# Optimization experiments

Measured on AMD Instinct MI355X. Metric: run time of the kernel, lower is better.

Reference implementation:

```python
import jax, jax.numpy as jnp
import numpy as np

HEADS = 16
EMBED = 1024
HEAD_DIM = EMBED // HEADS


def setup_inputs() -> dict:
    key = jax.random.key(0)
    ks = jax.random.split(key, 7)
    B, S, E = 2, 2048, EMBED
    scale = 1.0 / np.sqrt(E)
    return {
        "query": jax.random.normal(ks[0], (B, S, E), dtype=jnp.float32),
        "key": jax.random.normal(ks[1], (B, S, E), dtype=jnp.float32),
        "value": jax.random.normal(ks[2], (B, S, E), dtype=jnp.float32),
        # nn.Linear(E, E, bias=False) weights, applied as x @ W.T
        "Wq": jax.random.normal(ks[3], (E, E), dtype=jnp.float32) * scale,
        "Wk": jax.random.normal(ks[4], (E, E), dtype=jnp.float32) * scale,
        "Wv": jax.random.normal(ks[5], (E, E), dtype=jnp.float32) * scale,
        "Wo": jax.random.normal(ks[6], (E, E), dtype=jnp.float32) * scale,
    }


def reference(query, key, value, Wq, Wk, Wv, Wo):
    B, S, E = query.shape
    H, D = HEADS, HEAD_DIM

    def split_heads(x, W):
        # [B,S,E] @ W.T -> [B,S,E] -> [B,H,S,D]
        return (x @ W.T).reshape(B, -1, H, D).transpose(0, 2, 1, 3)

    q = split_heads(query, Wq)
    k = split_heads(key, Wk)
    v = split_heads(value, Wv)

    scores = jnp.einsum("bhqd,bhkd->bhqk", q, k) / jnp.sqrt(jnp.float32(D))
    attn = jax.nn.softmax(scores, axis=-1)  # [B,H,S,S]
    x = jnp.einsum("bhqk,bhkd->bhqd", attn, v)
    x = x.transpose(0, 2, 1, 3).reshape(B, -1, H * D)
    return x @ Wo.T
```

## Files before the change

kernel.cpp:

```cpp
#include <hip/hip_runtime.h>
#include <hip/hip_bf16.h>


typedef __attribute__((ext_vector_type(8))) short short8;
typedef __attribute__((ext_vector_type(4))) float f32x4;
typedef __attribute__((ext_vector_type(4))) unsigned short us4;
typedef __attribute__((ext_vector_type(4))) int i32x4;

#define MFMA16(a, b, c) __builtin_amdgcn_mfma_f32_16x16x32_bf16(a, b, c, 0, 0, 0)

static constexpr int B = 2;
static constexpr int S = 2048;
static constexpr int E = 1024;
static constexpr int H = 16;
static constexpr int D = 64;
static constexpr int M = B * S;
static constexpr size_t NE = (size_t)M * E;
static constexpr size_t NW = (size_t)E * E;

static __device__ __forceinline__ unsigned short f2bf(float x) {
  unsigned int u = __float_as_uint(x);
  unsigned int r = (u + 0x7FFFu + ((u >> 16) & 1u)) >> 16;
  return (unsigned short)r;
}

static __device__ __forceinline__ int cvt_pk_bf16(float lo, float hi) {
  int r;
  asm("v_cvt_pk_bf16_f32 %0, %1, %2" : "=v"(r) : "v"(lo), "v"(hi));
  return r;
}

static __device__ __forceinline__ void gload_lds16(const unsigned short* g,
                                                   unsigned short* l) {
  __builtin_amdgcn_global_load_lds(
      (const __attribute__((address_space(1))) unsigned int*)g,
      (__attribute__((address_space(3))) unsigned int*)l, 16, 0, 0);
}

__global__ void cvt_act_kernel(const float* __restrict__ s0,
                               const float* __restrict__ s1,
                               const float* __restrict__ s2,
                               unsigned short* __restrict__ d0,
                               unsigned short* __restrict__ d1,
                               unsigned short* __restrict__ d2, int n4) {
  const float* src = (blockIdx.y == 0) ? s0 : ((blockIdx.y == 1) ? s1 : s2);
  unsigned short* dst = (blockIdx.y == 0) ? d0 : ((blockIdx.y == 1) ? d1 : d2);
  for (int i = blockIdx.x * blockDim.x + threadIdx.x; i < n4;
       i += gridDim.x * blockDim.x) {
    float4 v = reinterpret_cast<const float4*>(src)[i];
    ushort4 o;
    o.x = f2bf(v.x); o.y = f2bf(v.y); o.z = f2bf(v.z); o.w = f2bf(v.w);
    reinterpret_cast<ushort4*>(dst)[i] = o;
  }
}

__global__ void cvt_w_kernel(const float* __restrict__ s0,
                             const float* __restrict__ s1,
                             const float* __restrict__ s2,
                             const float* __restrict__ s3,
                             unsigned short* __restrict__ d0,
                             unsigned short* __restrict__ d1,
                             unsigned short* __restrict__ d2,
                             unsigned short* __restrict__ d3, int n4) {
  const int z = blockIdx.y;
  const float* src = (z == 0) ? s0 : ((z == 1) ? s1 : ((z == 2) ? s2 : s3));
  unsigned short* dst = (z == 0) ? d0 : ((z == 1) ? d1 : ((z == 2) ? d2 : d3));
  for (int i = blockIdx.x * blockDim.x + threadIdx.x; i < n4;
       i += gridDim.x * blockDim.x) {
    float4 v = reinterpret_cast<const float4*>(src)[i];
    ushort4 o;
    o.x = f2bf(v.x); o.y = f2bf(v.y); o.z = f2bf(v.z); o.w = f2bf(v.w);
    reinterpret_cast<ushort4*>(dst)[i] = o;
  }
}

__global__ __launch_bounds__(256) void gemm_proj_kernel(
    const unsigned short* __restrict__ xq, const unsigned short* __restrict__ xk,
    const unsigned short* __restrict__ xv, const unsigned short* __restrict__ wq,
    const unsigned short* __restrict__ wk, const unsigned short* __restrict__ wv,
    unsigned short* __restrict__ Qh, unsigned short* __restrict__ Kh,
    unsigned short* __restrict__ Vt) {
  __shared__ __align__(16) unsigned short As[2][128 * 32];
  __shared__ __align__(16) unsigned short Bs[2][128 * 32];

  const int which = blockIdx.z;
  const unsigned short* A = (which == 0) ? xq : ((which == 1) ? xk : xv);
  const unsigned short* W = (which == 0) ? wq : ((which == 1) ? wk : wv);

  const int wave = threadIdx.x >> 6;
  const int lane = threadIdx.x & 63;
  const int lr = lane & 15;
  const int lk = (lane >> 4) * 8;
  const int m0 = blockIdx.x * 128;
  const int n0 = blockIdx.y * 128;
  const int wm = (wave >> 1) * 64;
  const int wn = (wave & 1) * 64;
  const int srow = lane >> 2;
  const int scol = (lane & 3) * 8;

  f32x4 acc[4][4];
  const f32x4 fz = {0.f, 0.f, 0.f, 0.f};
#pragma unroll
  for (int i = 0; i < 4; ++i)
#pragma unroll
    for (int j = 0; j < 4; ++j) acc[i][j] = fz;

#define STAGE_G(bb, kk)                                                       \
  {                                                                           \
    _Pragma("unroll") for (int i = 0; i < 2; ++i) {                           \
      const int c = wave * 2 + i;                                             \
      const int row = c * 16 + srow;                                          \
      gload_lds16(A + (size_t)(m0 + row) * E + (kk) + scol, &As[bb][c * 512]);\
      gload_lds16(W + (size_t)(n0 + row) * E + (kk) + scol, &Bs[bb][c * 512]);\
    }                                                                         \
  }

  STAGE_G(0, 0);
  __syncthreads();
  int buf = 0;
  for (int kk = 0; kk < E; kk += 32) {
    if (kk + 32 < E) STAGE_G(buf ^ 1, kk + 32);
    short8 af[4], bw[4];
#pragma unroll
    for (int i = 0; i < 4; ++i)
      af[i] = *reinterpret_cast<const short8*>(
          &As[buf][(wm + i * 16 + lr) * 32 + lk]);
#pragma unroll
    for (int j = 0; j < 4; ++j)
      bw[j] = *reinterpret_cast<const short8*>(
          &Bs[buf][(wn + j * 16 + lr) * 32 + lk]);
#pragma unroll
    for (int i = 0; i < 4; ++i)
#pragma unroll
      for (int j = 0; j < 4; ++j) acc[i][j] = MFMA16(af[i], bw[j], acc[i][j]);
    __syncthreads();
    buf ^= 1;
  }
#undef STAGE_G

  const int rbase = (lane >> 4) * 4;
#pragma unroll
  for (int i = 0; i < 4; ++i) {
#pragma unroll
    for (int j = 0; j < 4; ++j) {
      const int col = n0 + wn + j * 16 + lr;
      const int h = col >> 6, d = col & 63;
#pragma unroll
      for (int r = 0; r < 4; ++r) {
        const int row = m0 + wm + i * 16 + rbase + r;
        const int b = row >> 11, s = row & (S - 1);
        const float v = acc[i][j][r];
        if (which == 0) {
          Qh[(((size_t)b * H + h) * S + s) * D + d] = f2bf(v * 0.18033688f);
        } else if (which == 1) {
          Kh[(((size_t)b * H + h) * S + s) * D + d] = f2bf(v);
        } else {
          Vt[(((size_t)b * H + h) * D + d) * S + s] = f2bf(v);
        }
      }
    }
  }
}

__global__ __launch_bounds__(256) void gemm_out_kernel(
    const unsigned short* __restrict__ X, const unsigned short* __restrict__ Wo,
    float* __restrict__ out) {
  __shared__ __align__(16) unsigned short As[2][128 * 32];
  __shared__ __align__(16) unsigned short Bs[2][64 * 32];

  const int wave = threadIdx.x >> 6;
  const int lane = threadIdx.x & 63;
  const int lr = lane & 15;
  const int lk = (lane >> 4) * 8;
  const int m0 = blockIdx.x * 128;
  const int n0 = blockIdx.y * 64;
  const int wm = (wave >> 1) * 64;
  const int wn = (wave & 1) * 32;
  const int srow = lane >> 2;
  const int scol = (lane & 3) * 8;

  f32x4 acc[4][2];
  const f32x4 fz = {0.f, 0.f, 0.f, 0.f};
#pragma unroll
  for (int i = 0; i < 4; ++i)
#pragma unroll
    for (int j = 0; j < 2; ++j) acc[i][j] = fz;

#define STAGE_O(bb, kk)                                                       \
  {                                                                           \
    _Pragma("unroll") for (int i = 0; i < 2; ++i) {                           \
      const int c = wave * 2 + i;                                             \
      const int row = c * 16 + srow;                                          \
      gload_lds16(X + (size_t)(m0 + row) * E + (kk) + scol, &As[bb][c * 512]);\
    }                                                                         \
    gload_lds16(Wo + (size_t)(n0 + wave * 16 + srow) * E + (kk) + scol,       \
                &Bs[bb][wave * 512]);                                         \
  }

  STAGE_O(0, 0);
  __syncthreads();
  int buf = 0;
  for (int kk = 0; kk < E; kk += 32) {
    if (kk + 32 < E) STAGE_O(buf ^ 1, kk + 32);
    short8 af[4], bw[2];
#pragma unroll
    for (int i = 0; i < 4; ++i)
      af[i] = *reinterpret_cast<const short8*>(
          &As[buf][(wm + i * 16 + lr) * 32 + lk]);
#pragma unroll
    for (int j = 0; j < 2; ++j)
      bw[j] = *reinterpret_cast<const short8*>(
          &Bs[buf][(wn + j * 16 + lr) * 32 + lk]);
#pragma unroll
    for (int i = 0; i < 4; ++i)
#pragma unroll
      for (int j = 0; j < 2; ++j) acc[i][j] = MFMA16(af[i], bw[j], acc[i][j]);
    __syncthreads();
    buf ^= 1;
  }
#undef STAGE_O

  const int rbase = (lane >> 4) * 4;
#pragma unroll
  for (int i = 0; i < 4; ++i) {
#pragma unroll
    for (int j = 0; j < 2; ++j) {
      const int col = n0 + wn + j * 16 + lr;
#pragma unroll
      for (int r = 0; r < 4; ++r) {
        const int row = m0 + wm + i * 16 + rbase + r;
        out[(size_t)row * E + col] = acc[i][j][r];
      }
    }
  }
}

__global__ __launch_bounds__(256) void attn_kernel(
    const unsigned short* __restrict__ Qh, const unsigned short* __restrict__ Kh,
    const unsigned short* __restrict__ Vt, unsigned short* __restrict__ Xb) {
  __shared__ __align__(16) unsigned short Ks[2][64 * 64];
  __shared__ __align__(16) unsigned short Vs[2][64 * 64];

  const int wave = threadIdx.x >> 6;
  const int lane = threadIdx.x & 63;
  const int lr = lane & 15;
  const int jj = lane >> 4;
  const int lk = jj * 8;

  const int lin = blockIdx.x + (blockIdx.y << 5);
  const int nlin = (lin & 7) * 128 + (lin >> 3);
  const int qt = nlin & 31;
  const int bh = nlin >> 5;
  const int q0 = qt * 64 + wave * 16;

  const unsigned short* Qp = Qh + ((size_t)bh * S + q0) * D;
  short8 qf0 = *reinterpret_cast<const short8*>(Qp + (size_t)lr * D + lk);
  short8 qf1 = *reinterpret_cast<const short8*>(Qp + (size_t)lr * D + 32 + lk);

  const unsigned short* Kbase = Kh + (size_t)bh * S * D;
  const unsigned short* Vbase = Vt + (size_t)bh * D * S;

  const f32x4 fz = {0.f, 0.f, 0.f, 0.f};
  float mrun = -3.0e38f, lsum = 0.f;
  f32x4 acc[4];
#pragma unroll
  for (int dt = 0; dt < 4; ++dt) acc[dt] = fz;

  const int srow = lane >> 3;
  const int sgV = (lane & 7) ^ srow;

#define STAGE_KV(bb, kt)                                                      \
  {                                                                           \
    _Pragma("unroll") for (int i = 0; i < 2; ++i) {                           \
      const int c = wave * 2 + i;                                             \
      const int sgK = (lane & 7) ^ ((srow & 3) | ((c & 1) << 2));             \
      gload_lds16(Kbase + (size_t)((kt) + c * 8 + srow) * D + sgK * 8,        \
                  &Ks[bb][c * 512]);                                          \
      gload_lds16(Vbase + (size_t)(c * 8 + srow) * S + (kt) + sgV * 8,        \
                  &Vs[bb][c * 512]);                                          \
    }                                                                         \
  }

  STAGE_KV(0, 0);
  __syncthreads();
  int buf = 0;

  const int rb = ((lr >> 2) << 3) + (lr & 3);
  const int kswz = (lr & 3) | (((lr >> 2) & 1) << 2);
  const int vswz = lr & 7;

  constexpr int NT = S / 64;
  for (int t = 0; t < NT; ++t) {
    if (t + 1 < NT) STAGE_KV(buf ^ 1, (t + 1) * 64);

    f32x4 sf[4];
    __builtin_amdgcn_s_setprio(1);
#pragma unroll
    for (int nt = 0; nt < 4; ++nt) {
      const int r = rb + ((nt & 1) << 2) + ((nt >> 1) << 5);
      short8 kf0 = *reinterpret_cast<const short8*>(
          &Ks[buf][r * 64 + ((jj ^ kswz) * 8)]);
      short8 kf1 = *reinterpret_cast<const short8*>(
          &Ks[buf][r * 64 + (((jj + 4) ^ kswz) * 8)]);
      f32x4 z = fz;
      z = MFMA16(kf0, qf0, z);
      z = MFMA16(kf1, qf1, z);
      sf[nt] = z;
    }
    __builtin_amdgcn_s_setprio(0);

    short8 vf0[4], vf1[4];
#pragma unroll
    for (int dt = 0; dt < 4; ++dt) {
      const int r = dt * 16 + lr;
      vf0[dt] = *reinterpret_cast<const short8*>(
          &Vs[buf][r * 64 + ((jj ^ vswz) * 8)]);
      vf1[dt] = *reinterpret_cast<const short8*>(
          &Vs[buf][r * 64 + (((jj + 4) ^ vswz) * 8)]);
    }

    float mx = sf[0][0];
#pragma unroll
    for (int nt = 0; nt < 4; ++nt)
#pragma unroll
      for (int r = 0; r < 4; ++r) mx = fmaxf(mx, sf[nt][r]);
    mx = fmaxf(mx, __shfl_xor(mx, 16));
    mx = fmaxf(mx, __shfl_xor(mx, 32));

    if (__any(mx > mrun + 8.f)) {
      const float nm = fmaxf(mrun, mx);
      const float fac = __builtin_amdgcn_exp2f(mrun - nm);
      mrun = nm;
      lsum *= fac;
#pragma unroll
      for (int dt = 0; dt < 4; ++dt)
#pragma unroll
        for (int r = 0; r < 4; ++r) acc[dt][r] *= fac;
    }

    float p[4][4];
#pragma unroll
    for (int nt = 0; nt < 4; ++nt)
#pragma unroll
      for (int r = 0; r < 4; ++r) {
        p[nt][r] = __builtin_amdgcn_exp2f(sf[nt][r] - mrun);
        lsum += p[nt][r];
      }
    i32x4 w0, w1;
    w0.x = cvt_pk_bf16(p[0][0], p[0][1]);
    w0.y = cvt_pk_bf16(p[0][2], p[0][3]);
    w0.z = cvt_pk_bf16(p[1][0], p[1][1]);
    w0.w = cvt_pk_bf16(p[1][2], p[1][3]);
    w1.x = cvt_pk_bf16(p[2][0], p[2][1]);
    w1.y = cvt_pk_bf16(p[2][2], p[2][3]);
    w1.z = cvt_pk_bf16(p[3][0], p[3][1]);
    w1.w = cvt_pk_bf16(p[3][2], p[3][3]);
    short8 pa0 = __builtin_bit_cast(short8, w0);
    short8 pa1 = __builtin_bit_cast(short8, w1);

    __builtin_amdgcn_s_setprio(1);
#pragma unroll
    for (int dt = 0; dt < 4; ++dt) {
      acc[dt] = MFMA16(vf0[dt], pa0, acc[dt]);
      acc[dt] = MFMA16(vf1[dt], pa1, acc[dt]);
    }
    __builtin_amdgcn_s_setprio(0);

    __syncthreads();
    buf ^= 1;
  }
#undef STAGE_KV

  float ltot = lsum;
  ltot += __shfl_xor(ltot, 16);
  ltot += __shfl_xor(ltot, 32);
  const float inv = 1.0f / ltot;
  const int b = bh >> 4, h = bh & (H - 1);
  const int row = q0 + lr;
#pragma unroll
  for (int dt = 0; dt < 4; ++dt) {
    us4 o;
#pragma unroll
    for (int r = 0; r < 4; ++r) o[r] = f2bf(acc[dt][r] * inv);
    *reinterpret_cast<us4*>(
        &Xb[((size_t)b * S + row) * E + h * D + dt * 16 + 4 * jj]) = o;
  }
}

extern "C" void kernel_launch(void* const* d_in, const int* in_sizes, int n_in,
                              void* d_out, int out_size, void* d_ws, size_t ws_size,
                              hipStream_t stream) {
  const float* q_f = (const float*)d_in[0];
  const float* k_f = (const float*)d_in[1];
  const float* v_f = (const float*)d_in[2];
  const float* wq_f = (const float*)d_in[3];
  const float* wk_f = (const float*)d_in[4];
  const float* wv_f = (const float*)d_in[5];
  const float* wo_f = (const float*)d_in[6];

  unsigned short* xq = (unsigned short*)d_ws;
  unsigned short* xk = xq + NE;
  unsigned short* xv = xk + NE;
  unsigned short* wq = xv + NE;
  unsigned short* wk = wq + NW;
  unsigned short* wv = wk + NW;
  unsigned short* wo = wv + NW;
  unsigned short* Qh = wo + NW;
  unsigned short* Kh = Qh + NE;
  unsigned short* Vt = Kh + NE;
  unsigned short* Xb = Vt + NE;

  cvt_act_kernel<<<dim3(512, 3), 256, 0, stream>>>(q_f, k_f, v_f, xq, xk, xv,
                                                   (int)(NE / 4));
  cvt_w_kernel<<<dim3(256, 4), 256, 0, stream>>>(wq_f, wk_f, wv_f, wo_f, wq, wk,
                                                 wv, wo, (int)(NW / 4));

  gemm_proj_kernel<<<dim3(M / 128, E / 128, 3), 256, 0, stream>>>(
      xq, xk, xv, wq, wk, wv, Qh, Kh, Vt);

  attn_kernel<<<dim3(S / 64, B * H), 256, 0, stream>>>(Qh, Kh, Vt, Xb);

  gemm_out_kernel<<<dim3(M / 128, E / 64), 256, 0, stream>>>(Xb, wo,
                                                             (float*)d_out);
}
```

Before: 159.5 us.

## Process two 16-row query tiles per wave in attention to reuse K/V fragments

Each wave of the attention kernel now handles 32 query rows as two independent 16-row tiles, so the block covers 128 queries and the grid in x is halved. K and V fragments read from LDS are reused across both tiles, and the global K/V staging per query row is also halved. Each tile keeps its own softmax state. The cost is roughly double the accumulator and score registers and only 512 blocks, which may lower occupancy and the number of waves in flight.

```diff
diff --git a/kernel.cpp b/kernel.cpp
--- a/kernel.cpp
+++ b/kernel.cpp
@@ -247,24 +247,28 @@
   const int jj = lane >> 4;
   const int lk = jj * 8;
 
-  const int lin = blockIdx.x + (blockIdx.y << 5);
-  const int nlin = (lin & 7) * 128 + (lin >> 3);
-  const int qt = nlin & 31;
-  const int bh = nlin >> 5;
-  const int q0 = qt * 64 + wave * 16;
-
-  const unsigned short* Qp = Qh + ((size_t)bh * S + q0) * D;
-  short8 qf0 = *reinterpret_cast<const short8*>(Qp + (size_t)lr * D + lk);
-  short8 qf1 = *reinterpret_cast<const short8*>(Qp + (size_t)lr * D + 32 + lk);
+  const int lin = blockIdx.x + (blockIdx.y << 4);
+  const int nlin = (lin & 7) * 64 + (lin >> 3);
+  const int qt = nlin & 15;
+  const int bh = nlin >> 4;
+  const int q0 = qt * 128 + wave * 32;
+
+  const unsigned short* Qp0 = Qh + ((size_t)bh * S + q0) * D;
+  const unsigned short* Qp1 = Qp0 + (size_t)16 * D;
+  short8 qa0 = *reinterpret_cast<const short8*>(Qp0 + (size_t)lr * D + lk);
+  short8 qa1 = *reinterpret_cast<const short8*>(Qp0 + (size_t)lr * D + 32 + lk);
+  short8 qb0 = *reinterpret_cast<const short8*>(Qp1 + (size_t)lr * D + lk);
+  short8 qb1 = *reinterpret_cast<const short8*>(Qp1 + (size_t)lr * D + 32 + lk);
 
   const unsigned short* Kbase = Kh + (size_t)bh * S * D;
   const unsigned short* Vbase = Vt + (size_t)bh * D * S;
 
   const f32x4 fz = {0.f, 0.f, 0.f, 0.f};
-  float mrun = -3.0e38f, lsum = 0.f;
-  f32x4 acc[4];
-#pragma unroll
-  for (int dt = 0; dt < 4; ++dt) acc[dt] = fz;
+  float mrunA = -3.0e38f, lsumA = 0.f;
+  float mrunB = -3.0e38f, lsumB = 0.f;
+  f32x4 accA[4], accB[4];
+#pragma unroll
+  for (int dt = 0; dt < 4; ++dt) { accA[dt] = fz; accB[dt] = fz; }
 
   const int srow = lane >> 3;
   const int sgV = (lane & 7) ^ srow;
@@ -293,7 +297,7 @@
   for (int t = 0; t < NT; ++t) {
     if (t + 1 < NT) STAGE_KV(buf ^ 1, (t + 1) * 64);
 
-    f32x4 sf[4];
+    f32x4 sfA[4], sfB[4];
     __builtin_amdgcn_s_setprio(1);
 #pragma unroll
     for (int nt = 0; nt < 4; ++nt) {
@@ -302,10 +306,13 @@
           &Ks[buf][r * 64 + ((jj ^ kswz) * 8)]);
       short8 kf1 = *reinterpret_cast<const short8*>(
           &Ks[buf][r * 64 + (((jj + 4) ^ kswz) * 8)]);
-      f32x4 z = fz;
-      z = MFMA16(kf0, qf0, z);
-      z = MFMA16(kf1, qf1, z);
-      sf[nt] = z;
+      f32x4 za = fz, zb = fz;
+      za = MFMA16(kf0, qa0, za);
+      za = MFMA16(kf1, qa1, za);
+      zb = MFMA16(kf0, qb0, zb);
+      zb = MFMA16(kf1, qb1, zb);
+      sfA[nt] = za;
+      sfB[nt] = zb;
     }
     __builtin_amdgcn_s_setprio(0);
 
@@ -319,50 +326,87 @@
           &Vs[buf][r * 64 + (((jj + 4) ^ vswz) * 8)]);
     }
 
-    float mx = sf[0][0];
+    float mxA = sfA[0][0];
 #pragma unroll
     for (int nt = 0; nt < 4; ++nt)
 #pragma unroll
-      for (int r = 0; r < 4; ++r) mx = fmaxf(mx, sf[nt][r]);
-    mx = fmaxf(mx, __shfl_xor(mx, 16));
-    mx = fmaxf(mx, __shfl_xor(mx, 32));
-
-    if (__any(mx > mrun + 8.f)) {
-      const float nm = fmaxf(mrun, mx);
-      const float fac = __builtin_amdgcn_exp2f(mrun - nm);
-      mrun = nm;
-      lsum *= fac;
+      for (int r = 0; r < 4; ++r) mxA = fmaxf(mxA, sfA[nt][r]);
+    mxA = fmaxf(mxA, __shfl_xor(mxA, 16));
+    mxA = fmaxf(mxA, __shfl_xor(mxA, 32));
+    if (__any(mxA > mrunA + 8.f)) {
+      const float nm = fmaxf(mrunA, mxA);
+      const float fac = __builtin_amdgcn_exp2f(mrunA - nm);
+      mrunA = nm;
+      lsumA *= fac;
 #pragma unroll
       for (int dt = 0; dt < 4; ++dt)
 #pragma unroll
-        for (int r = 0; r < 4; ++r) acc[dt][r] *= fac;
-    }
-
-    float p[4][4];
+        for (int r = 0; r < 4; ++r) accA[dt][r] *= fac;
+    }
+    float pA[4][4];
 #pragma unroll
     for (int nt = 0; nt < 4; ++nt)
 #pragma unroll
       for (int r = 0; r < 4; ++r) {
-        p[nt][r] = __builtin_amdgcn_exp2f(sf[nt][r] - mrun);
-        lsum += p[nt][r];
+        pA[nt][r] = __builtin_amdgcn_exp2f(sfA[nt][r] - mrunA);
+        lsumA += pA[nt][r];
       }
-    i32x4 w0, w1;
-    w0.x = cvt_pk_bf16(p[0][0], p[0][1]);
-    w0.y = cvt_pk_bf16(p[0][2], p[0][3]);
-    w0.z = cvt_pk_bf16(p[1][0], p[1][1]);
-    w0.w = cvt_pk_bf16(p[1][2], p[1][3]);
-    w1.x = cvt_pk_bf16(p[2][0], p[2][1]);
-    w1.y = cvt_pk_bf16(p[2][2], p[2][3]);
-    w1.z = cvt_pk_bf16(p[3][0], p[3][1]);
-    w1.w = cvt_pk_bf16(p[3][2], p[3][3]);
-    short8 pa0 = __builtin_bit_cast(short8, w0);
-    short8 pa1 = __builtin_bit_cast(short8, w1);
+    i32x4 wa0, wa1;
+    wa0.x = cvt_pk_bf16(pA[0][0], pA[0][1]);
+    wa0.y = cvt_pk_bf16(pA[0][2], pA[0][3]);
+    wa0.z = cvt_pk_bf16(pA[1][0], pA[1][1]);
+    wa0.w = cvt_pk_bf16(pA[1][2], pA[1][3]);
+    wa1.x = cvt_pk_bf16(pA[2][0], pA[2][1]);
+    wa1.y = cvt_pk_bf16(pA[2][2], pA[2][3]);
+    wa1.z = cvt_pk_bf16(pA[3][0], pA[3][1]);
+    wa1.w = cvt_pk_bf16(pA[3][2], pA[3][3]);
+    short8 paA0 = __builtin_bit_cast(short8, wa0);
+    short8 paA1 = __builtin_bit_cast(short8, wa1);
+
+    float mxB = sfB[0][0];
+#pragma unroll
+    for (int nt = 0; nt < 4; ++nt)
+#pragma unroll
+      for (int r = 0; r < 4; ++r) mxB = fmaxf(mxB, sfB[nt][r]);
+    mxB = fmaxf(mxB, __shfl_xor(mxB, 16));
+    mxB = fmaxf(mxB, __shfl_xor(mxB, 32));
+    if (__any(mxB > mrunB + 8.f)) {
+      const float nm = fmaxf(mrunB, mxB);
+      const float fac = __builtin_amdgcn_exp2f(mrunB - nm);
+      mrunB = nm;
+      lsumB *= fac;
+#pragma unroll
+      for (int dt = 0; dt < 4; ++dt)
+#pragma unroll
+        for (int r = 0; r < 4; ++r) accB[dt][r] *= fac;
+    }
+    float pB[4][4];
+#pragma unroll
+    for (int nt = 0; nt < 4; ++nt)
+#pragma unroll
+      for (int r = 0; r < 4; ++r) {
+        pB[nt][r] = __builtin_amdgcn_exp2f(sfB[nt][r] - mrunB);
+        lsumB += pB[nt][r];
+      }
+    i32x4 wb0, wb1;
+    wb0.x = cvt_pk_bf16(pB[0][0], pB[0][1]);
+    wb0.y = cvt_pk_bf16(pB[0][2], pB[0][3]);
+    wb0.z = cvt_pk_bf16(pB[1][0], pB[1][1]);
+    wb0.w = cvt_pk_bf16(pB[1][2], pB[1][3]);
+    wb1.x = cvt_pk_bf16(pB[2][0], pB[2][1]);
+    wb1.y = cvt_pk_bf16(pB[2][2], pB[2][3]);
+    wb1.z = cvt_pk_bf16(pB[3][0], pB[3][1]);
+    wb1.w = cvt_pk_bf16(pB[3][2], pB[3][3]);
+    short8 paB0 = __builtin_bit_cast(short8, wb0);
+    short8 paB1 = __builtin_bit_cast(short8, wb1);
 
     __builtin_amdgcn_s_setprio(1);
 #pragma unroll
     for (int dt = 0; dt < 4; ++dt) {
-      acc[dt] = MFMA16(vf0[dt], pa0, acc[dt]);
-      acc[dt] = MFMA16(vf1[dt], pa1, acc[dt]);
+      accA[dt] = MFMA16(vf0[dt], paA0, accA[dt]);
+      accA[dt] = MFMA16(vf1[dt], paA1, accA[dt]);
+      accB[dt] = MFMA16(vf0[dt], paB0, accB[dt]);
+      accB[dt] = MFMA16(vf1[dt], paB1, accB[dt]);
     }
     __builtin_amdgcn_s_setprio(0);
 
@@ -371,19 +415,36 @@
   }
 #undef STAGE_KV
 
-  float ltot = lsum;
-  ltot += __shfl_xor(ltot, 16);
-  ltot += __shfl_xor(ltot, 32);
-  const float inv = 1.0f / ltot;
   const int b = bh >> 4, h = bh & (H - 1);
-  const int row = q0 + lr;
-#pragma unroll
-  for (int dt = 0; dt < 4; ++dt) {
-    us4 o;
-#pragma unroll
-    for (int r = 0; r < 4; ++r) o[r] = f2bf(acc[dt][r] * inv);
-    *reinterpret_cast<us4*>(
-        &Xb[((size_t)b * S + row) * E + h * D + dt * 16 + 4 * jj]) = o;
+  {
+    float ltot = lsumA;
+    ltot += __shfl_xor(ltot, 16);
+    ltot += __shfl_xor(ltot, 32);
+    const float inv = 1.0f / ltot;
+    const int row = q0 + lr;
+#pragma unroll
+    for (int dt = 0; dt < 4; ++dt) {
+      us4 o;
+#pragma unroll
+      for (int r = 0; r < 4; ++r) o[r] = f2bf(accA[dt][r] * inv);
+      *reinterpret_cast<us4*>(
+          &Xb[((size_t)b * S + row) * E + h * D + dt * 16 + 4 * jj]) = o;
+    }
+  }
+  {
+    float ltot = lsumB;
+    ltot += __shfl_xor(ltot, 16);
+    ltot += __shfl_xor(ltot, 32);
+    const float inv = 1.0f / ltot;
+    const int row = q0 + 16 + lr;
+#pragma unroll
+    for (int dt = 0; dt < 4; ++dt) {
+      us4 o;
+#pragma unroll
+      for (int r = 0; r < 4; ++r) o[r] = f2bf(accB[dt][r] * inv);
+      *reinterpret_cast<us4*>(
+          &Xb[((size_t)b * S + row) * E + h * D + dt * 16 + 4 * jj]) = o;
+    }
   }
 }
 
@@ -418,7 +479,7 @@
   gemm_proj_kernel<<<dim3(M / 128, E / 128, 3), 256, 0, stream>>>(
       xq, xk, xv, wq, wk, wv, Qh, Kh, Vt);
 
-  attn_kernel<<<dim3(S / 64, B * H), 256, 0, stream>>>(Qh, Kh, Vt, Xb);
+  attn_kernel<<<dim3(S / 128, B * H), 256, 0, stream>>>(Qh, Kh, Vt, Xb);
 
   gemm_out_kernel<<<dim3(M / 128, E / 64), 256, 0, stream>>>(Xb, wo,
                                                              (float*)d_out);
```

Result: faster. 145.4 us (-8.8%).

## Give each attention wave four query tiles to reuse K/V fragments; merge conversion kernels

Applied to the files above, without the earlier changes.

The attention kernel now runs 2 waves per block, each handling 64 query rows (four 16-row groups) instead of 16. K and V fragments loaded from LDS are reused across the four query groups, which cuts LDS reads per unit of MFMA work and halves the number of blocks. The trade-off is more registers per wave (four sets of accumulators and softmax state), which lowers occupancy, and a grid of 512 blocks. Separately, the activation and weight fp32-to-bf16 conversions are merged into one launch to save a kernel launch.

```diff
diff --git a/kernel.cpp b/kernel.cpp
--- a/kernel.cpp
+++ b/kernel.cpp
@@ -37,34 +37,27 @@
       (__attribute__((address_space(3))) unsigned int*)l, 16, 0, 0);
 }
 
-__global__ void cvt_act_kernel(const float* __restrict__ s0,
+__global__ void cvt_all_kernel(const float* __restrict__ s0,
                                const float* __restrict__ s1,
                                const float* __restrict__ s2,
+                               const float* __restrict__ s3,
+                               const float* __restrict__ s4,
+                               const float* __restrict__ s5,
+                               const float* __restrict__ s6,
                                unsigned short* __restrict__ d0,
                                unsigned short* __restrict__ d1,
-                               unsigned short* __restrict__ d2, int n4) {
-  const float* src = (blockIdx.y == 0) ? s0 : ((blockIdx.y == 1) ? s1 : s2);
-  unsigned short* dst = (blockIdx.y == 0) ? d0 : ((blockIdx.y == 1) ? d1 : d2);
-  for (int i = blockIdx.x * blockDim.x + threadIdx.x; i < n4;
-       i += gridDim.x * blockDim.x) {
-    float4 v = reinterpret_cast<const float4*>(src)[i];
-    ushort4 o;
-    o.x = f2bf(v.x); o.y = f2bf(v.y); o.z = f2bf(v.z); o.w = f2bf(v.w);
-    reinterpret_cast<ushort4*>(dst)[i] = o;
-  }
-}
-
-__global__ void cvt_w_kernel(const float* __restrict__ s0,
-                             const float* __restrict__ s1,
-                             const float* __restrict__ s2,
-                             const float* __restrict__ s3,
-                             unsigned short* __restrict__ d0,
-                             unsigned short* __restrict__ d1,
-                             unsigned short* __restrict__ d2,
-                             unsigned short* __restrict__ d3, int n4) {
+                               unsigned short* __restrict__ d2,
+                               unsigned short* __restrict__ d3,
+                               unsigned short* __restrict__ d4,
+                               unsigned short* __restrict__ d5,
+                               unsigned short* __restrict__ d6, int nAct4,
+                               int nW4) {
   const int z = blockIdx.y;
-  const float* src = (z == 0) ? s0 : ((z == 1) ? s1 : ((z == 2) ? s2 : s3));
-  unsigned short* dst = (z == 0) ? d0 : ((z == 1) ? d1 : ((z == 2) ? d2 : d3));
+  const float* srcs[7] = {s0, s1, s2, s3, s4, s5, s6};
+  unsigned short* dsts[7] = {d0, d1, d2, d3, d4, d5, d6};
+  const float* src = srcs[z];
+  unsigned short* dst = dsts[z];
+  const int n4 = (z < 3) ? nAct4 : nW4;
   for (int i = blockIdx.x * blockDim.x + threadIdx.x; i < n4;
        i += gridDim.x * blockDim.x) {
     float4 v = reinterpret_cast<const float4*>(src)[i];
@@ -235,7 +228,7 @@
   }
 }
 
-__global__ __launch_bounds__(256) void attn_kernel(
+__global__ __launch_bounds__(128) void attn_kernel(
     const unsigned short* __restrict__ Qh, const unsigned short* __restrict__ Kh,
     const unsigned short* __restrict__ Vt, unsigned short* __restrict__ Xb) {
   __shared__ __align__(16) unsigned short Ks[2][64 * 64];
@@ -247,32 +240,41 @@
   const int jj = lane >> 4;
   const int lk = jj * 8;
 
-  const int lin = blockIdx.x + (blockIdx.y << 5);
-  const int nlin = (lin & 7) * 128 + (lin >> 3);
-  const int qt = nlin & 31;
-  const int bh = nlin >> 5;
-  const int q0 = qt * 64 + wave * 16;
-
-  const unsigned short* Qp = Qh + ((size_t)bh * S + q0) * D;
-  short8 qf0 = *reinterpret_cast<const short8*>(Qp + (size_t)lr * D + lk);
-  short8 qf1 = *reinterpret_cast<const short8*>(Qp + (size_t)lr * D + 32 + lk);
+  const int lin = blockIdx.x + (blockIdx.y << 4);
+  const int nlin = (lin & 7) * 64 + (lin >> 3);
+  const int qt = nlin & 15;
+  const int bh = nlin >> 4;
+  const int q0 = qt * 128 + wave * 64;
+
+  short8 qf[4][2];
+#pragma unroll
+  for (int g = 0; g < 4; ++g) {
+    const unsigned short* Qp = Qh + ((size_t)bh * S + q0 + g * 16) * D;
+    qf[g][0] = *reinterpret_cast<const short8*>(Qp + (size_t)lr * D + lk);
+    qf[g][1] = *reinterpret_cast<const short8*>(Qp + (size_t)lr * D + 32 + lk);
+  }
 
   const unsigned short* Kbase = Kh + (size_t)bh * S * D;
   const unsigned short* Vbase = Vt + (size_t)bh * D * S;
 
   const f32x4 fz = {0.f, 0.f, 0.f, 0.f};
-  float mrun = -3.0e38f, lsum = 0.f;
-  f32x4 acc[4];
-#pragma unroll
-  for (int dt = 0; dt < 4; ++dt) acc[dt] = fz;
+  float mrun[4], lsum[4];
+  f32x4 acc[4][4];
+#pragma unroll
+  for (int g = 0; g < 4; ++g) {
+    mrun[g] = -3.0e38f;
+    lsum[g] = 0.f;
+#pragma unroll
+    for (int dt = 0; dt < 4; ++dt) acc[g][dt] = fz;
+  }
 
   const int srow = lane >> 3;
   const int sgV = (lane & 7) ^ srow;
 
 #define STAGE_KV(bb, kt)                                                      \
   {                                                                           \
-    _Pragma("unroll") for (int i = 0; i < 2; ++i) {                           \
-      const int c = wave * 2 + i;                                             \
+    _Pragma("unroll") for (int i = 0; i < 4; ++i) {                           \
+      const int c = wave * 4 + i;                                             \
       const int sgK = (lane & 7) ^ ((srow & 3) | ((c & 1) << 2));             \
       gload_lds16(Kbase + (size_t)((kt) + c * 8 + srow) * D + sgK * 8,        \
                   &Ks[bb][c * 512]);                                          \
@@ -293,23 +295,15 @@
   for (int t = 0; t < NT; ++t) {
     if (t + 1 < NT) STAGE_KV(buf ^ 1, (t + 1) * 64);
 
-    f32x4 sf[4];
-    __builtin_amdgcn_s_setprio(1);
+    short8 kf0[4], kf1[4], vf0[4], vf1[4];
 #pragma unroll
     for (int nt = 0; nt < 4; ++nt) {
       const int r = rb + ((nt & 1) << 2) + ((nt >> 1) << 5);
-      short8 kf0 = *reinterpret_cast<const short8*>(
+      kf0[nt] = *reinterpret_cast<const short8*>(
           &Ks[buf][r * 64 + ((jj ^ kswz) * 8)]);
-      short8 kf1 = *reinterpret_cast<const short8*>(
+      kf1[nt] = *reinterpret_cast<const short8*>(
           &Ks[buf][r * 64 + (((jj + 4) ^ kswz) * 8)]);
-      f32x4 z = fz;
-      z = MFMA16(kf0, qf0, z);
-      z = MFMA16(kf1, qf1, z);
-      sf[nt] = z;
-    }
-    __builtin_amdgcn_s_setprio(0);
-
-    short8 vf0[4], vf1[4];
+    }
 #pragma unroll
     for (int dt = 0; dt < 4; ++dt) {
       const int r = dt * 16 + lr;
@@ -319,71 +313,87 @@
           &Vs[buf][r * 64 + (((jj + 4) ^ vswz) * 8)]);
     }
 
-    float mx = sf[0][0];
-#pragma unroll
-    for (int nt = 0; nt < 4; ++nt)
-#pragma unroll
-      for (int r = 0; r < 4; ++r) mx = fmaxf(mx, sf[nt][r]);
-    mx = fmaxf(mx, __shfl_xor(mx, 16));
-    mx = fmaxf(mx, __shfl_xor(mx, 32));
-
-    if (__any(mx > mrun + 8.f)) {
-      const float nm = fmaxf(mrun, mx);
-      const float fac = __builtin_amdgcn_exp2f(mrun - nm);
-      mrun = nm;
-      lsum *= fac;
-#pragma unroll
-      for (int dt = 0; dt < 4; ++dt)
-#pragma unroll
-        for (int r = 0; r < 4; ++r) acc[dt][r] *= fac;
-    }
-
-    float p[4][4];
-#pragma unroll
-    for (int nt = 0; nt < 4; ++nt)
-#pragma unroll
-      for (int r = 0; r < 4; ++r) {
-        p[nt][r] = __builtin_amdgcn_exp2f(sf[nt][r] - mrun);
-        lsum += p[nt][r];
+#pragma unroll
+    for (int g = 0; g < 4; ++g) {
+      f32x4 sf[4];
+      __builtin_amdgcn_s_setprio(1);
+#pragma unroll
+      for (int nt = 0; nt < 4; ++nt) {
+        f32x4 z = fz;
+        z = MFMA16(kf0[nt], qf[g][0], z);
+        z = MFMA16(kf1[nt], qf[g][1], z);
+        sf[nt] = z;
       }
-    i32x4 w0, w1;
-    w0.x = cvt_pk_bf16(p[0][0], p[0][1]);
-    w0.y = cvt_pk_bf16(p[0][2], p[0][3]);
-    w0.z = cvt_pk_bf16(p[1][0], p[1][1]);
-    w0.w = cvt_pk_bf16(p[1][2], p[1][3]);
-    w1.x = cvt_pk_bf16(p[2][0], p[2][1]);
-    w1.y = cvt_pk_bf16(p[2][2], p[2][3]);
-    w1.z = cvt_pk_bf16(p[3][0], p[3][1]);
-    w1.w = cvt_pk_bf16(p[3][2], p[3][3]);
-    short8 pa0 = __builtin_bit_cast(short8, w0);
-    short8 pa1 = __builtin_bit_cast(short8, w1);
-
-    __builtin_amdgcn_s_setprio(1);
-#pragma unroll
-    for (int dt = 0; dt < 4; ++dt) {
-      acc[dt] = MFMA16(vf0[dt], pa0, acc[dt]);
-      acc[dt] = MFMA16(vf1[dt], pa1, acc[dt]);
-    }
-    __builtin_amdgcn_s_setprio(0);
+      __builtin_amdgcn_s_setprio(0);
+
+      float mx = sf[0][0];
+#pragma unroll
+      for (int nt = 0; nt < 4; ++nt)
+#pragma unroll
+        for (int r = 0; r < 4; ++r) mx = fmaxf(mx, sf[nt][r]);
+      mx = fmaxf(mx, __shfl_xor(mx, 16));
+      mx = fmaxf(mx, __shfl_xor(mx, 32));
+
+      if (__any(mx > mrun[g] + 8.f)) {
+        const float nm = fmaxf(mrun[g], mx);
+        const float fac = __builtin_amdgcn_exp2f(mrun[g] - nm);
+        mrun[g] = nm;
+        lsum[g] *= fac;
+#pragma unroll
+        for (int dt = 0; dt < 4; ++dt)
+#pragma unroll
+          for (int r = 0; r < 4; ++r) acc[g][dt][r] *= fac;
+      }
+
+#pragma unroll
+      for (int nt = 0; nt < 4; ++nt)
+#pragma unroll
+        for (int r = 0; r < 4; ++r) {
+          sf[nt][r] = __builtin_amdgcn_exp2f(sf[nt][r] - mrun[g]);
+          lsum[g] += sf[nt][r];
+        }
+      i32x4 w0, w1;
+      w0.x = cvt_pk_bf16(sf[0][0], sf[0][1]);
+      w0.y = cvt_pk_bf16(sf[0][2], sf[0][3]);
+      w0.z = cvt_pk_bf16(sf[1][0], sf[1][1]);
+      w0.w = cvt_pk_bf16(sf[1][2], sf[1][3]);
+      w1.x = cvt_pk_bf16(sf[2][0], sf[2][1]);
+      w1.y = cvt_pk_bf16(sf[2][2], sf[2][3]);
+      w1.z = cvt_pk_bf16(sf[3][0], sf[3][1]);
+      w1.w = cvt_pk_bf16(sf[3][2], sf[3][3]);
+      const short8 pa0 = __builtin_bit_cast(short8, w0);
+      const short8 pa1 = __builtin_bit_cast(short8, w1);
+
+      __builtin_amdgcn_s_setprio(1);
+#pragma unroll
+      for (int dt = 0; dt < 4; ++dt) {
+        acc[g][dt] = MFMA16(vf0[dt], pa0, acc[g][dt]);
+        acc[g][dt] = MFMA16(vf1[dt], pa1, acc[g][dt]);
+      }
+      __builtin_amdgcn_s_setprio(0);
+    }
 
     __syncthreads();
     buf ^= 1;
   }
 #undef STAGE_KV
 
-  float ltot = lsum;
-  ltot += __shfl_xor(ltot, 16);
-  ltot += __shfl_xor(ltot, 32);
-  const float inv = 1.0f / ltot;
   const int b = bh >> 4, h = bh & (H - 1);
-  const int row = q0 + lr;
-#pragma unroll
-  for (int dt = 0; dt < 4; ++dt) {
-    us4 o;
-#pragma unroll
-    for (int r = 0; r < 4; ++r) o[r] = f2bf(acc[dt][r] * inv);
-    *reinterpret_cast<us4*>(
-        &Xb[((size_t)b * S + row) * E + h * D + dt * 16 + 4 * jj]) = o;
+#pragma unroll
+  for (int g = 0; g < 4; ++g) {
+    float ltot = lsum[g];
+    ltot += __shfl_xor(ltot, 16);
+    ltot += __shfl_xor(ltot, 32);
+    const float inv = 1.0f / ltot;
+    const int row = q0 + g * 16 + lr;
+#pragma unroll
+    for (int dt = 0; dt < 4; ++dt) {
+      us4 o;
+#pragma unroll
+      for (int r = 0; r < 4; ++r) o[r] = f2bf(acc[g][dt][r] * inv);
+      *reinterpret_cast<us4*>(
+          &Xb[((size_t)b * S + row) * E + h * D + dt * 16 + 4 * jj]) = o;
+    }
   }
 }
 
@@ -410,15 +420,14 @@
   unsigned short* Vt = Kh + NE;
   unsigned short* Xb = Vt + NE;
 
-  cvt_act_kernel<<<dim3(512, 3), 256, 0, stream>>>(q_f, k_f, v_f, xq, xk, xv,
-                                                   (int)(NE / 4));
-  cvt_w_kernel<<<dim3(256, 4), 256, 0, stream>>>(wq_f, wk_f, wv_f, wo_f, wq, wk,
-                                                 wv, wo, (int)(NW / 4));
+  cvt_all_kernel<<<dim3(512, 7), 256, 0, stream>>>(
+      q_f, k_f, v_f, wq_f, wk_f, wv_f, wo_f, xq, xk, xv, wq, wk, wv, wo,
+      (int)(NE / 4), (int)(NW / 4));
 
   gemm_proj_kernel<<<dim3(M / 128, E / 128, 3), 256, 0, stream>>>(
       xq, xk, xv, wq, wk, wv, Qh, Kh, Vt);
 
-  attn_kernel<<<dim3(S / 64, B * H), 256, 0, stream>>>(Qh, Kh, Vt, Xb);
+  attn_kernel<<<dim3(S / 128, B * H), 128, 0, stream>>>(Qh, Kh, Vt, Xb);
 
   gemm_out_kernel<<<dim3(M / 128, E / 64), 256, 0, stream>>>(Xb, wo,
                                                              (float*)d_out);
```

Result: slower. 163.3 us (+2.4%).
